# Kernel optimization log

Measured on AMD Instinct MI355X. Metric: run time of the kernel, lower is better.

## Reference

```python
import jax, jax.numpy as jnp
import numpy as np

N, E, D, H = 50000, 800000, 64, 4  # nodes, edges, hidden_dim (=edge_hidden_dim=out), heads
NEG_SLOPE = 0.2  # DGL EGATConv leaky_relu default


def setup_inputs() -> dict:
    key = jax.random.key(0)
    ks = jax.random.split(key, 12)
    s = 1.0 / np.sqrt(D)
    sm = 1.0 / np.sqrt(H * D)
    return {
        "h_E": jax.random.normal(ks[0], (N, D), jnp.float32),      # node feats
        "h_H": jax.random.normal(ks[1], (E, D), jnp.float32),      # edge feats
        "src": jax.random.randint(ks[2], (E,), 0, N),
        "dst": jax.random.randint(ks[3], (E,), 0, N),
        "W_node": jax.random.normal(ks[4], (D, H * D), jnp.float32) * s,
        "b_node": jnp.zeros((H * D,), jnp.float32),
        "W_ni": jax.random.normal(ks[5], (D, H * D), jnp.float32) * s,
        "W_nj": jax.random.normal(ks[6], (D, H * D), jnp.float32) * s,
        "W_fij": jax.random.normal(ks[7], (D, H * D), jnp.float32) * s,
        "attn": jax.random.normal(ks[8], (H, D), jnp.float32) * s,
        "Wp_node": jax.random.normal(ks[9], (H * D, D), jnp.float32) * sm,
        "bp_node": jnp.zeros((D,), jnp.float32),
        "Wp_edge": jax.random.normal(ks[10], (H * D, D), jnp.float32) * sm,
        "bp_edge": jnp.zeros((D,), jnp.float32),
    }


def reference(h_E, h_H, src, dst, W_node, b_node, W_ni, W_nj, W_fij, attn,
              Wp_node, bp_node, Wp_edge, bp_edge):
    # EGAT edge update: f_ij = LeakyReLU(fc_ni(h_i) + fc_nj(h_j) + fc_fij(e_ij))
    f = (h_E @ W_ni)[src] + (h_E @ W_nj)[dst] + h_H @ W_fij          # (E, H*D)
    f = jax.nn.leaky_relu(f, NEG_SLOPE).reshape(E, H, D)
    # per-head attention logit and edge-softmax grouped by destination node
    e = jnp.einsum('ehd,hd->eh', f, attn)                            # (E, H)
    emax = jax.ops.segment_max(e, dst, num_segments=N)               # (N, H)
    a = jnp.exp(e - emax[dst])
    a = a / jax.ops.segment_sum(a, dst, num_segments=N)[dst]         # (E, H)
    # attention-weighted aggregation of projected source nodes
    h_proj = (h_E @ W_node + b_node).reshape(N, H, D)
    agg = jax.ops.segment_sum(h_proj[src] * a[:, :, None], dst, num_segments=N)  # (N, H, D)
    # merge heads back to hidden dims, then residual add
    hE_new = agg.reshape(N, H * D) @ Wp_node + bp_node
    hH_new = f.reshape(E, H * D) @ Wp_edge + bp_edge
    return h_E + hE_new, h_H + hH_new
```

## Files before the change

### kernel.cpp

```cpp
#include <hip/hip_runtime.h>
#include <math.h>

#define NEG_SLOPE 0.2f

typedef __bf16 bf16x8 __attribute__((ext_vector_type(8)));
typedef float f32x4 __attribute__((ext_vector_type(4)));
typedef float f32x4v __attribute__((ext_vector_type(4)));

__device__ __forceinline__ ushort f2bf(float x) {
  union { float f; unsigned u; } v; v.f = x;
  unsigned r = v.u + 0x7fffu + ((v.u >> 16) & 1u);
  return (ushort)(r >> 16);
}
__device__ __forceinline__ float bf2f(ushort b) {
  union { unsigned u; float f; } v; v.u = (unsigned)b << 16;
  return v.f;
}

__device__ __forceinline__ int swz(int m) {
  return ((m & 7) << 4) | (((m >> 3) & 3) << 7);
}

__global__ void k_prep(const float* __restrict__ Wfij,
                       const float* __restrict__ Wni,
                       const float* __restrict__ Wnj,
                       const float* __restrict__ Wpe,
                       ushort* __restrict__ WcatT, ushort* __restrict__ WpeT) {
  int i = blockIdx.x * 256 + threadIdx.x;
  if (i < 49152) {
    int c = i / 192, k = i % 192;
    float v = (k < 64) ? Wfij[k * 256 + c]
            : (k < 128) ? Wni[(k - 64) * 256 + c]
                        : Wnj[(k - 128) * 256 + c];
    WcatT[c * 192 + k] = f2bf(v);
  }
  if (i < 16384) {
    int k2 = i >> 6, n2 = i & 63;
    WpeT[n2 * 256 + k2] = f2bf(Wpe[i]);
  }
}

__global__ __launch_bounds__(256) void k_node(
    const float* __restrict__ hE,
    const float* __restrict__ Wnode, const float* __restrict__ bnode,
    const float* __restrict__ Wpn,
    ushort* __restrict__ hE_bf, ushort* __restrict__ hq, int n) {
  __shared__ float hEt[64 * 36];
  __shared__ float hpl[32 * 260];
  const int tid = threadIdx.x;
  const int n0 = blockIdx.x * 32;

#pragma unroll
  for (int i = 0; i < 8; ++i) {
    int flat = tid + i * 256;
    int m = flat >> 6, k = flat & 63;
    float v = (n0 + m < n) ? hE[(size_t)(n0 + m) * 64 + k] : 0.f;
    hEt[k * 36 + m] = v;
    if (n0 + m < n) hE_bf[(size_t)(n0 + m) * 64 + k] = f2bf(v);
  }
  __syncthreads();

  const int tm = tid >> 5, tc = tid & 31, c0 = tc * 8;

  {
    float acc[4][8];
#pragma unroll
    for (int mm = 0; mm < 4; ++mm)
#pragma unroll
      for (int j = 0; j < 8; ++j) acc[mm][j] = 0.f;

    for (int k = 0; k < 64; ++k) {
      float4 h4 = *(const float4*)&hEt[k * 36 + tm * 4];
      float4 w0 = *(const float4*)&Wnode[k * 256 + c0];
      float4 w1 = *(const float4*)&Wnode[k * 256 + c0 + 4];
      float hv[4] = {h4.x, h4.y, h4.z, h4.w};
      float wv[8] = {w0.x, w0.y, w0.z, w0.w, w1.x, w1.y, w1.z, w1.w};
#pragma unroll
      for (int mm = 0; mm < 4; ++mm)
#pragma unroll
        for (int j = 0; j < 8; ++j) acc[mm][j] += hv[mm] * wv[j];
    }
#pragma unroll
    for (int mm = 0; mm < 4; ++mm) {
      int m = tm * 4 + mm;
#pragma unroll
      for (int j = 0; j < 8; ++j)
        hpl[m * 260 + c0 + j] = acc[mm][j] + bnode[c0 + j];
    }
  }
  __syncthreads();

  const int hh = tc >> 3, dc0 = (tc & 7) * 8;
  float acc[4][8];
#pragma unroll
  for (int mm = 0; mm < 4; ++mm)
#pragma unroll
    for (int j = 0; j < 8; ++j) acc[mm][j] = 0.f;

  for (int k = 0; k < 64; ++k) {
    float4 w0 = *(const float4*)&Wpn[(size_t)(hh * 64 + k) * 64 + dc0];
    float4 w1 = *(const float4*)&Wpn[(size_t)(hh * 64 + k) * 64 + dc0 + 4];
    float wv[8] = {w0.x, w0.y, w0.z, w0.w, w1.x, w1.y, w1.z, w1.w};
#pragma unroll
    for (int mm = 0; mm < 4; ++mm) {
      float hv = hpl[(tm * 4 + mm) * 260 + hh * 64 + k];
#pragma unroll
      for (int j = 0; j < 8; ++j) acc[mm][j] += hv * wv[j];
    }
  }
#pragma unroll
  for (int mm = 0; mm < 4; ++mm) {
    int m = tm * 4 + mm;
    if (n0 + m < n) {
      ushort u[8];
#pragma unroll
      for (int j = 0; j < 8; ++j) u[j] = f2bf(acc[mm][j]);
      *(uint4*)&hq[(size_t)(n0 + m) * 256 + c0] = *(const uint4*)u;
    }
  }
}

__global__ void k_zero(int* __restrict__ deg, int n) {
  int g = blockIdx.x * 256 + threadIdx.x;
  if (g < n) deg[g] = 0;
}

__global__ void k_hist(const int* __restrict__ dst, int* __restrict__ deg,
                       int E) {
  int g = blockIdx.x * 256 + threadIdx.x;
  if (g < E) atomicAdd(&deg[dst[g]], 1);
}

__global__ __launch_bounds__(1024) void k_scanA(const int* __restrict__ deg,
                                                int* __restrict__ off,
                                                int* __restrict__ btot, int n) {
  __shared__ int sbuf[1024];
  int t = threadIdx.x, g = blockIdx.x * 1024 + t;
  int v = (g < n) ? deg[g] : 0;
  sbuf[t] = v;
  __syncthreads();
  for (int ofs = 1; ofs < 1024; ofs <<= 1) {
    int x = (t >= ofs) ? sbuf[t - ofs] : 0;
    __syncthreads();
    sbuf[t] += x;
    __syncthreads();
  }
  if (g < n) off[g] = sbuf[t] - v;
  if (t == 1023) btot[blockIdx.x] = sbuf[t];
}

__global__ void k_scanB(const int* __restrict__ btot, int* __restrict__ boff,
                        int nb) {
  if (threadIdx.x == 0 && blockIdx.x == 0) {
    int acc = 0;
    for (int b = 0; b < nb; ++b) { boff[b] = acc; acc += btot[b]; }
  }
}

__global__ void k_scanC(int* __restrict__ off, const int* __restrict__ boff,
                        int* __restrict__ cursor, int n, int E) {
  int g = blockIdx.x * 1024 + threadIdx.x;
  if (g < n) {
    int v = off[g] + boff[g >> 10];
    off[g] = v;
    cursor[g] = v;
  }
  if (g == n) off[n] = E;
}

__global__ void k_scatter(const int* __restrict__ dst,
                          const int* __restrict__ src,
                          int* __restrict__ cursor, int* __restrict__ rank,
                          int* __restrict__ srcs, int E) {
  int g = blockIdx.x * 256 + threadIdx.x;
  if (g < E) {
    int pos = atomicAdd(&cursor[dst[g]], 1);
    rank[g] = pos;
    srcs[pos] = src[g];
  }
}

__global__ __launch_bounds__(256, 2) void k_edge(
    const float* __restrict__ hH,
    const int* __restrict__ src, const int* __restrict__ dst,
    const ushort* __restrict__ WcatT,
    const float* __restrict__ attn,
    const ushort* __restrict__ WpeT,
    const float* __restrict__ bpe,
    const ushort* __restrict__ hE_bf,
    const int* __restrict__ rank,
    float* __restrict__ e_ws,
    float* __restrict__ out1, int ntiles) {
  __shared__ __align__(16) char smem[32 * 384 + 32 * 512 + 128];
  char* ab = smem;
  char* fb = smem + 12288;
  int* rkbuf = (int*)(smem + 28672);

  const int tid = threadIdx.x;
  const int w = tid >> 6, l = tid & 63;
  const int lr = l & 15, lk = l >> 4;
  const int swa = (lr & 7) << 4;
  const int stm = tid >> 3, sts = tid & 7;
  const int swm = (stm & 7) << 4;

  bf16x8 bw1[6][4];
#pragma unroll
  for (int ks = 0; ks < 6; ++ks)
#pragma unroll
    for (int nt = 0; nt < 4; ++nt)
      bw1[ks][nt] = *(const bf16x8*)(WcatT +
          (size_t)(w * 64 + nt * 16 + lr) * 192 + ks * 32 + lk * 8);
  bf16x8 bw2[8];
#pragma unroll
  for (int ks = 0; ks < 8; ++ks)
    bw2[ks] = *(const bf16x8*)(WpeT +
        (size_t)(w * 16 + lr) * 256 + ks * 32 + lk * 8);
  float av[4];
#pragma unroll
  for (int nt = 0; nt < 4; ++nt) av[nt] = attn[w * 64 + nt * 16 + lr];
  const float bpv = bpe[w * 16 + lr];
  const int sw0 = swz(lr), sw1 = swz(16 + lr);

  for (int tile = blockIdx.x; tile < ntiles; tile += gridDim.x) {
    const int e0 = tile * 32;

    if (tid < 32) rkbuf[tid] = rank[e0 + tid];
    {
      int sn = src[e0 + stm], dn = dst[e0 + stm];
      char* arow = ab + stm * 384;
      const f32x4v* p =
          (const f32x4v*)(hH + (size_t)(e0 + stm) * 64 + sts * 8);
      f32x4v x = __builtin_nontemporal_load(p);
      f32x4v y = __builtin_nontemporal_load(p + 1);
      ushort u[8] = {f2bf(x[0]), f2bf(x[1]), f2bf(x[2]), f2bf(x[3]),
                     f2bf(y[0]), f2bf(y[1]), f2bf(y[2]), f2bf(y[3])};
      *(uint4*)(arow + ((sts * 16) ^ swm)) = *(const uint4*)u;
      *(uint4*)(arow + (128 + ((sts * 16) ^ swm))) =
          *(const uint4*)(hE_bf + (size_t)sn * 64 + sts * 8);
      *(uint4*)(arow + (256 + ((sts * 16) ^ swm))) =
          *(const uint4*)(hE_bf + (size_t)dn * 64 + sts * 8);
    }
    __syncthreads();

    f32x4 acc[2][4];
#pragma unroll
    for (int mt = 0; mt < 2; ++mt)
#pragma unroll
      for (int nt = 0; nt < 4; ++nt) acc[mt][nt] = (f32x4){0.f, 0.f, 0.f, 0.f};

#pragma unroll
    for (int ks = 0; ks < 6; ++ks) {
      int sec = (ks >> 1) << 7;
      int off = ((ks & 1) << 6) | (lk << 4);
      bf16x8 a0 = *(const bf16x8*)(ab + lr * 384 + sec + (off ^ swa));
      bf16x8 a1 = *(const bf16x8*)(ab + (16 + lr) * 384 + sec + (off ^ swa));
#pragma unroll
      for (int nt = 0; nt < 4; ++nt) {
        acc[0][nt] = __builtin_amdgcn_mfma_f32_16x16x32_bf16(
            a0, bw1[ks][nt], acc[0][nt], 0, 0, 0);
        acc[1][nt] = __builtin_amdgcn_mfma_f32_16x16x32_bf16(
            a1, bw1[ks][nt], acc[1][nt], 0, 0, 0);
      }
    }

    float pkeep[2][4];
#pragma unroll
    for (int mt = 0; mt < 2; ++mt) {
#pragma unroll
      for (int r = 0; r < 4; ++r) {
        int m = mt * 16 + lk * 4 + r;
        char* rowp = fb + m * 512;
        int sw = swz(m);
        float p = 0.f;
#pragma unroll
        for (int nt = 0; nt < 4; ++nt) {
          int c = w * 64 + nt * 16 + lr;
          float v = acc[mt][nt][r];
          v = (v >= 0.f) ? v : NEG_SLOPE * v;
          p += v * av[nt];
          *(ushort*)(rowp + ((c * 2) ^ sw)) = f2bf(v);
        }
        p += __shfl_xor(p, 1);
        p += __shfl_xor(p, 2);
        p += __shfl_xor(p, 4);
        p += __shfl_xor(p, 8);
        pkeep[mt][r] = p;
      }
    }
    __syncthreads();

    f32x4 acc2[2];
    acc2[0] = (f32x4){0.f, 0.f, 0.f, 0.f};
    acc2[1] = (f32x4){0.f, 0.f, 0.f, 0.f};
#pragma unroll
    for (int ks = 0; ks < 8; ++ks) {
      int ko = (ks * 32 + lk * 8) * 2;
      bf16x8 a0 = *(const bf16x8*)(fb + lr * 512 + (ko ^ sw0));
      bf16x8 a1 = *(const bf16x8*)(fb + (16 + lr) * 512 + (ko ^ sw1));
      acc2[0] =
          __builtin_amdgcn_mfma_f32_16x16x32_bf16(a0, bw2[ks], acc2[0], 0, 0, 0);
      acc2[1] =
          __builtin_amdgcn_mfma_f32_16x16x32_bf16(a1, bw2[ks], acc2[1], 0, 0, 0);
    }

#pragma unroll
    for (int mt = 0; mt < 2; ++mt)
#pragma unroll
      for (int r = 0; r < 4; ++r) {
        int m = mt * 16 + lk * 4 + r;
        int swmr = (m & 7) << 4;
        ushort h =
            *(const ushort*)(ab + m * 384 + ((((w * 16 + lr) * 2)) ^ swmr));
        size_t idx = (size_t)(e0 + m) * 64 + w * 16 + lr;
        __builtin_nontemporal_store(acc2[mt][r] + bf2f(h) + bpv, &out1[idx]);
      }
    if (lr == 0) {
#pragma unroll
      for (int mt = 0; mt < 2; ++mt)
#pragma unroll
        for (int r = 0; r < 4; ++r) {
          int m = mt * 16 + lk * 4 + r;
          e_ws[(size_t)rkbuf[m] * 4 + w] = pkeep[mt][r];
        }
    }
    __syncthreads();
  }
}

__global__ __launch_bounds__(256) void k3_csr(
    const int* __restrict__ csr_off, const float* __restrict__ e_ws,
    const int* __restrict__ srcs, const ushort* __restrict__ hq,
    const float* __restrict__ hE, const float* __restrict__ bpn,
    float* __restrict__ out0, int n) {
  int node = blockIdx.x * 4 + (threadIdx.x >> 6);
  if (node >= n) return;
  int d = threadIdx.x & 63;
  int beg = csr_off[node], end = csr_off[node + 1];
  float base = hE[(size_t)node * 64 + d] + bpn[d];
  if (beg == end) {
    out0[(size_t)node * 64 + d] = base;
    return;
  }
  float s0 = 0.f, s1 = 0.f, s2 = 0.f, s3 = 0.f;
  float y0 = 0.f, y1 = 0.f, y2 = 0.f, y3 = 0.f;
  for (int i = beg; i < end; ++i) {
    f32x4 ev = *(const f32x4*)(e_ws + (size_t)i * 4);
    int sn = srcs[i];
    float w0 = __expf(ev[0] - 12.f);
    float w1 = __expf(ev[1] - 12.f);
    float w2 = __expf(ev[2] - 12.f);
    float w3 = __expf(ev[3] - 12.f);
    s0 += w0; s1 += w1; s2 += w2; s3 += w3;
    const ushort* hp = hq + (size_t)sn * 256;
    y0 += w0 * bf2f(hp[d]);
    y1 += w1 * bf2f(hp[64 + d]);
    y2 += w2 * bf2f(hp[128 + d]);
    y3 += w3 * bf2f(hp[192 + d]);
  }
  float y = y0 / s0 + y1 / s1 + y2 / s2 + y3 / s3;
  out0[(size_t)node * 64 + d] = base + y;
}

extern "C" void kernel_launch(void* const* d_in, const int* in_sizes, int n_in,
                              void* d_out, int out_size, void* d_ws, size_t ws_size,
                              hipStream_t stream) {
  const float* h_E    = (const float*)d_in[0];
  const float* h_H    = (const float*)d_in[1];
  const int*   src    = (const int*)d_in[2];
  const int*   dst    = (const int*)d_in[3];
  const float* W_node = (const float*)d_in[4];
  const float* b_node = (const float*)d_in[5];
  const float* W_ni   = (const float*)d_in[6];
  const float* W_nj   = (const float*)d_in[7];
  const float* W_fij  = (const float*)d_in[8];
  const float* attn   = (const float*)d_in[9];
  const float* Wp_node= (const float*)d_in[10];
  const float* bp_node= (const float*)d_in[11];
  const float* Wp_edge= (const float*)d_in[12];
  const float* bp_edge= (const float*)d_in[13];

  const int n = in_sizes[0] / 64;
  const int e = in_sizes[1] / 64;
  const int nscan = (n + 1023) / 1024;

  ushort* ws_hEbf = (ushort*)d_ws;
  ushort* ws_hq   = ws_hEbf + (size_t)n * 64;
  float*  ws_e    = (float*)(ws_hq + (size_t)n * 256);
  int*    ws_deg  = (int*)(ws_e + (size_t)e * 4);
  int*    ws_off  = ws_deg + n;
  int*    ws_cur  = ws_off + n + 1;
  int*    ws_btot = ws_cur + n;
  int*    ws_boff = ws_btot + 64;
  int*    ws_rank = ws_boff + 64;
  int*    ws_srcs = ws_rank + e;
  ushort* ws_Wcat = (ushort*)(ws_srcs + e);
  ushort* ws_WpeT = ws_Wcat + 49152;

  float* out0 = (float*)d_out;
  float* out1 = out0 + (size_t)n * 64;

  k_prep<<<192, 256, 0, stream>>>(W_fij, W_ni, W_nj, Wp_edge, ws_Wcat, ws_WpeT);
  {
    int blocks = (n + 31) / 32;
    k_node<<<blocks, 256, 0, stream>>>(h_E, W_node, b_node, Wp_node,
                                       ws_hEbf, ws_hq, n);
  }
  k_zero<<<(n + 255) / 256, 256, 0, stream>>>(ws_deg, n);
  k_hist<<<(e + 255) / 256, 256, 0, stream>>>(dst, ws_deg, e);
  k_scanA<<<nscan, 1024, 0, stream>>>(ws_deg, ws_off, ws_btot, n);
  k_scanB<<<1, 64, 0, stream>>>(ws_btot, ws_boff, nscan);
  k_scanC<<<nscan, 1024, 0, stream>>>(ws_off, ws_boff, ws_cur, n, e);
  k_scatter<<<(e + 255) / 256, 256, 0, stream>>>(dst, src, ws_cur, ws_rank,
                                                 ws_srcs, e);
  {
    int ntiles = e / 32;
    k_edge<<<1024, 256, 0, stream>>>(h_H, src, dst, ws_Wcat, attn, ws_WpeT,
                                     bp_edge, ws_hEbf, ws_rank, ws_e, out1,
                                     ntiles);
  }
  {
    int blocks = (n + 3) / 4;
    k3_csr<<<blocks, 256, 0, stream>>>(ws_off, ws_e, ws_srcs, ws_hq, h_E,
                                       bp_node, out0, n);
  }
}
```

Measured before the change: 462.8 us.

## Fuse small setup kernels, use native bf16 conversion, unroll CSR aggregation

Folds the degree-zeroing into the weight prep kernel and merges the single-thread block-offset scan into the final scan pass, which removes two kernel launches. Swaps the manual float-to-bf16 rounding for native __bf16 casts in the node and edge kernels. Unrolls the per-node CSR aggregation loop by four with separate accumulators so more gather loads can be in flight at once. The extra accumulators raise register use, and each scanC block now sums the preceding block totals serially (at most about 49 values).

```diff
diff --git a/kernel.cpp b/kernel.cpp
--- a/kernel.cpp
+++ b/kernel.cpp
@@ -25,7 +25,8 @@
                        const float* __restrict__ Wni,
                        const float* __restrict__ Wnj,
                        const float* __restrict__ Wpe,
-                       ushort* __restrict__ WcatT, ushort* __restrict__ WpeT) {
+                       ushort* __restrict__ WcatT, ushort* __restrict__ WpeT,
+                       int* __restrict__ deg, int n) {
   int i = blockIdx.x * 256 + threadIdx.x;
   if (i < 49152) {
     int c = i / 192, k = i % 192;
@@ -38,6 +39,7 @@
     int k2 = i >> 6, n2 = i & 63;
     WpeT[n2 * 256 + k2] = f2bf(Wpe[i]);
   }
+  if (i < n) deg[i] = 0;
 }
 
 __global__ __launch_bounds__(256) void k_node(
@@ -112,17 +114,12 @@
   for (int mm = 0; mm < 4; ++mm) {
     int m = tm * 4 + mm;
     if (n0 + m < n) {
-      ushort u[8];
-#pragma unroll
-      for (int j = 0; j < 8; ++j) u[j] = f2bf(acc[mm][j]);
-      *(uint4*)&hq[(size_t)(n0 + m) * 256 + c0] = *(const uint4*)u;
-    }
-  }
-}
-
-__global__ void k_zero(int* __restrict__ deg, int n) {
-  int g = blockIdx.x * 256 + threadIdx.x;
-  if (g < n) deg[g] = 0;
+      bf16x8 u;
+#pragma unroll
+      for (int j = 0; j < 8; ++j) u[j] = (__bf16)acc[mm][j];
+      *(bf16x8*)&hq[(size_t)(n0 + m) * 256 + c0] = u;
+    }
+  }
 }
 
 __global__ void k_hist(const int* __restrict__ dst, int* __restrict__ deg,
@@ -149,19 +146,20 @@
   if (t == 1023) btot[blockIdx.x] = sbuf[t];
 }
 
-__global__ void k_scanB(const int* __restrict__ btot, int* __restrict__ boff,
-                        int nb) {
-  if (threadIdx.x == 0 && blockIdx.x == 0) {
+__global__ __launch_bounds__(1024) void k_scanC(int* __restrict__ off,
+                                                const int* __restrict__ btot,
+                                                int* __restrict__ cursor,
+                                                int n, int E) {
+  __shared__ int carry;
+  if (threadIdx.x == 0) {
     int acc = 0;
-    for (int b = 0; b < nb; ++b) { boff[b] = acc; acc += btot[b]; }
-  }
-}
-
-__global__ void k_scanC(int* __restrict__ off, const int* __restrict__ boff,
-                        int* __restrict__ cursor, int n, int E) {
+    for (int b = 0; b < (int)blockIdx.x; ++b) acc += btot[b];
+    carry = acc;
+  }
+  __syncthreads();
   int g = blockIdx.x * 1024 + threadIdx.x;
   if (g < n) {
-    int v = off[g] + boff[g >> 10];
+    int v = off[g] + carry;
     off[g] = v;
     cursor[g] = v;
   }
@@ -232,9 +230,12 @@
           (const f32x4v*)(hH + (size_t)(e0 + stm) * 64 + sts * 8);
       f32x4v x = __builtin_nontemporal_load(p);
       f32x4v y = __builtin_nontemporal_load(p + 1);
-      ushort u[8] = {f2bf(x[0]), f2bf(x[1]), f2bf(x[2]), f2bf(x[3]),
-                     f2bf(y[0]), f2bf(y[1]), f2bf(y[2]), f2bf(y[3])};
-      *(uint4*)(arow + ((sts * 16) ^ swm)) = *(const uint4*)u;
+      bf16x8 u;
+      u[0] = (__bf16)x[0]; u[1] = (__bf16)x[1];
+      u[2] = (__bf16)x[2]; u[3] = (__bf16)x[3];
+      u[4] = (__bf16)y[0]; u[5] = (__bf16)y[1];
+      u[6] = (__bf16)y[2]; u[7] = (__bf16)y[3];
+      *(bf16x8*)(arow + ((sts * 16) ^ swm)) = u;
       *(uint4*)(arow + (128 + ((sts * 16) ^ swm))) =
           *(const uint4*)(hE_bf + (size_t)sn * 64 + sts * 8);
       *(uint4*)(arow + (256 + ((sts * 16) ^ swm))) =
@@ -278,7 +279,7 @@
           float v = acc[mt][nt][r];
           v = (v >= 0.f) ? v : NEG_SLOPE * v;
           p += v * av[nt];
-          *(ushort*)(rowp + ((c * 2) ^ sw)) = f2bf(v);
+          *(__bf16*)(rowp + ((c * 2) ^ sw)) = (__bf16)v;
         }
         p += __shfl_xor(p, 1);
         p += __shfl_xor(p, 2);
@@ -341,24 +342,42 @@
     out0[(size_t)node * 64 + d] = base;
     return;
   }
-  float s0 = 0.f, s1 = 0.f, s2 = 0.f, s3 = 0.f;
-  float y0 = 0.f, y1 = 0.f, y2 = 0.f, y3 = 0.f;
-  for (int i = beg; i < end; ++i) {
+  float s[4][4] = {};
+  float y[4][4] = {};
+  int i = beg;
+  for (; i + 3 < end; i += 4) {
+#pragma unroll
+    for (int u = 0; u < 4; ++u) {
+      f32x4 ev = *(const f32x4*)(e_ws + (size_t)(i + u) * 4);
+      const ushort* hp = hq + (size_t)srcs[i + u] * 256;
+      float w0 = __expf(ev[0] - 12.f), w1 = __expf(ev[1] - 12.f);
+      float w2 = __expf(ev[2] - 12.f), w3 = __expf(ev[3] - 12.f);
+      s[u][0] += w0; s[u][1] += w1; s[u][2] += w2; s[u][3] += w3;
+      y[u][0] += w0 * bf2f(hp[d]);
+      y[u][1] += w1 * bf2f(hp[64 + d]);
+      y[u][2] += w2 * bf2f(hp[128 + d]);
+      y[u][3] += w3 * bf2f(hp[192 + d]);
+    }
+  }
+  for (; i < end; ++i) {
     f32x4 ev = *(const f32x4*)(e_ws + (size_t)i * 4);
-    int sn = srcs[i];
-    float w0 = __expf(ev[0] - 12.f);
-    float w1 = __expf(ev[1] - 12.f);
-    float w2 = __expf(ev[2] - 12.f);
-    float w3 = __expf(ev[3] - 12.f);
-    s0 += w0; s1 += w1; s2 += w2; s3 += w3;
-    const ushort* hp = hq + (size_t)sn * 256;
-    y0 += w0 * bf2f(hp[d]);
-    y1 += w1 * bf2f(hp[64 + d]);
-    y2 += w2 * bf2f(hp[128 + d]);
-    y3 += w3 * bf2f(hp[192 + d]);
-  }
-  float y = y0 / s0 + y1 / s1 + y2 / s2 + y3 / s3;
-  out0[(size_t)node * 64 + d] = base + y;
+    const ushort* hp = hq + (size_t)srcs[i] * 256;
+    float w0 = __expf(ev[0] - 12.f), w1 = __expf(ev[1] - 12.f);
+    float w2 = __expf(ev[2] - 12.f), w3 = __expf(ev[3] - 12.f);
+    s[0][0] += w0; s[0][1] += w1; s[0][2] += w2; s[0][3] += w3;
+    y[0][0] += w0 * bf2f(hp[d]);
+    y[0][1] += w1 * bf2f(hp[64 + d]);
+    y[0][2] += w2 * bf2f(hp[128 + d]);
+    y[0][3] += w3 * bf2f(hp[192 + d]);
+  }
+  float out = base;
+#pragma unroll
+  for (int h = 0; h < 4; ++h) {
+    float sh = s[0][h] + s[1][h] + s[2][h] + s[3][h];
+    float yh = y[0][h] + y[1][h] + y[2][h] + y[3][h];
+    out += yh / sh;
+  }
+  out0[(size_t)node * 64 + d] = out;
 }
 
 extern "C" void kernel_launch(void* const* d_in, const int* in_sizes, int n_in,
@@ -390,8 +409,7 @@
   int*    ws_off  = ws_deg + n;
   int*    ws_cur  = ws_off + n + 1;
   int*    ws_btot = ws_cur + n;
-  int*    ws_boff = ws_btot + 64;
-  int*    ws_rank = ws_boff + 64;
+  int*    ws_rank = ws_btot + 64;
   int*    ws_srcs = ws_rank + e;
   ushort* ws_Wcat = (ushort*)(ws_srcs + e);
   ushort* ws_WpeT = ws_Wcat + 49152;
@@ -399,17 +417,16 @@
   float* out0 = (float*)d_out;
   float* out1 = out0 + (size_t)n * 64;
 
-  k_prep<<<192, 256, 0, stream>>>(W_fij, W_ni, W_nj, Wp_edge, ws_Wcat, ws_WpeT);
+  k_prep<<<196, 256, 0, stream>>>(W_fij, W_ni, W_nj, Wp_edge, ws_Wcat,
+                                  ws_WpeT, ws_deg, n);
   {
     int blocks = (n + 31) / 32;
     k_node<<<blocks, 256, 0, stream>>>(h_E, W_node, b_node, Wp_node,
                                        ws_hEbf, ws_hq, n);
   }
-  k_zero<<<(n + 255) / 256, 256, 0, stream>>>(ws_deg, n);
   k_hist<<<(e + 255) / 256, 256, 0, stream>>>(dst, ws_deg, e);
   k_scanA<<<nscan, 1024, 0, stream>>>(ws_deg, ws_off, ws_btot, n);
-  k_scanB<<<1, 64, 0, stream>>>(ws_btot, ws_boff, nscan);
-  k_scanC<<<nscan, 1024, 0, stream>>>(ws_off, ws_boff, ws_cur, n, e);
+  k_scanC<<<nscan, 1024, 0, stream>>>(ws_off, ws_btot, ws_cur, n, e);
   k_scatter<<<(e + 255) / 256, 256, 0, stream>>>(dst, src, ws_cur, ws_rank,
                                                  ws_srcs, e);
   {
```

After: 450.7 us. 2.6% less time.
